# Kernel optimization log

Hardware: AMD Instinct MI355X
Metric: run time of the kernel (lower is better)

Reference implementation:

```python
import jax, jax.numpy as jnp
import numpy as np

N_NODES = 100000
N_EDGES = 1600000
IN_DIM = 128
HEADS = 2
OUT_DIM = 64


def setup_inputs() -> dict:
    key = jax.random.key(0)
    k1, k2, k3, k4, k5 = jax.random.split(key, 5)
    x = jax.random.normal(k1, (N_NODES, IN_DIM), dtype=jnp.float32)
    edge_index = jax.random.randint(k2, (2, N_EDGES), 0, N_NODES, dtype=jnp.int32)
    # xavier-uniform-ish scales
    W = jax.random.uniform(k3, (IN_DIM, HEADS * OUT_DIM), dtype=jnp.float32,
                           minval=-1.0, maxval=1.0) * (6.0 / (IN_DIM + HEADS * OUT_DIM)) ** 0.5
    attn_l = jax.random.uniform(k4, (HEADS, OUT_DIM), dtype=jnp.float32,
                                minval=-1.0, maxval=1.0) * (6.0 / (HEADS + OUT_DIM)) ** 0.5
    attn_r = jax.random.uniform(k5, (HEADS, OUT_DIM), dtype=jnp.float32,
                                minval=-1.0, maxval=1.0) * (6.0 / (HEADS + OUT_DIM)) ** 0.5
    return {"x": x, "edge_index": edge_index, "W": W, "attn_l": attn_l, "attn_r": attn_r}


def reference(x, edge_index, W, attn_l, attn_r):
    N = x.shape[0]
    h = (x @ W).reshape(N, HEADS, OUT_DIM)          # [N,H,D]
    src, dst = edge_index[0], edge_index[1]          # [E]
    h_src = h[src]                                   # [E,H,D] gather
    h_dst = h[dst]                                   # [E,H,D] gather
    # per-edge, per-head attention logits
    alpha = jnp.einsum('ehd,hd->eh', h_src, attn_l) + jnp.einsum('ehd,hd->eh', h_dst, attn_r)
    alpha = jax.nn.leaky_relu(alpha, negative_slope=0.2)
    # NOTE: faithful to original torch code: softmax over dim=0 (ALL edges per head)
    alpha = jax.nn.softmax(alpha, axis=0)            # [E,H]
    msg = h_src * alpha[:, :, None]                  # [E,H,D]
    out = jnp.zeros((N, HEADS, OUT_DIM), dtype=h.dtype).at[dst].add(msg)
    return out.reshape(N, HEADS * OUT_DIM)
```

## Files before the change

### kernel.cpp

```cpp
#include <hip/hip_runtime.h>
#include <hip/hip_fp16.h>
#include <math.h>

#define IN_DIM   128
#define HEADS    2
#define OUT_DIM  64
#define OCOLS    128
#define NB_A     1024
#define BSHIFT   8
#define MAXB     512
#define PCOPIES  8
#define CAP      6144
#define PARTB    128
#define LOG2E    1.4426950408889634f

typedef __attribute__((ext_vector_type(4))) _Float16 half4v;
typedef __attribute__((ext_vector_type(8))) _Float16 half8v;
typedef __attribute__((ext_vector_type(4))) float    floatx4;

__global__ __launch_bounds__(256) void pack_w_kernel(
    const float* __restrict__ W, half8v* __restrict__ wpack) {
  int t = threadIdx.x;
  for (int s = t; s < 2048; s += 256) {
    int l = s & 63, ct = (s >> 6) & 7, kk = s >> 9;
    int q = l >> 4, n = l & 15;
    int c = ct * 16 + n;
    half8v f;
#pragma unroll
    for (int j = 0; j < 8; j++) {
      f[j] = (_Float16)W[(size_t)(kk * 32 + q * 8 + j) * OCOLS + c];
    }
    wpack[s] = f;
  }
}

__global__ __launch_bounds__(256) void gemm_kernel(
    const float* __restrict__ x, const half8v* __restrict__ wpack,
    const float* __restrict__ attn_l, const float* __restrict__ attn_r,
    _Float16* __restrict__ h16, float* __restrict__ alr, int N) {
  __shared__ half8v Wlds[2048];
  __shared__ __align__(16) _Float16 hstage[64 * OCOLS];
  const int tid = threadIdx.x;
  for (int i = tid; i < 2048; i += 256) Wlds[i] = wpack[i];

  const int wave = tid >> 6, lane = tid & 63;
  const int q = lane >> 4, m = lane & 15;
  const int rbase = blockIdx.x * 64 + wave * 16;
  const int arow = rbase + m;
  const bool rok = arow < N;

  half8v a[4];
#pragma unroll
  for (int kk = 0; kk < 4; kk++) {
    float4 u = rok ? *(const float4*)&x[(size_t)arow * IN_DIM + kk * 32 + q * 8]
                   : make_float4(0.f, 0.f, 0.f, 0.f);
    float4 v = rok ? *(const float4*)&x[(size_t)arow * IN_DIM + kk * 32 + q * 8 + 4]
                   : make_float4(0.f, 0.f, 0.f, 0.f);
    a[kk][0] = (_Float16)u.x; a[kk][1] = (_Float16)u.y;
    a[kk][2] = (_Float16)u.z; a[kk][3] = (_Float16)u.w;
    a[kk][4] = (_Float16)v.x; a[kk][5] = (_Float16)v.y;
    a[kk][6] = (_Float16)v.z; a[kk][7] = (_Float16)v.w;
  }
  __syncthreads();

  floatx4 acc[8];
#pragma unroll
  for (int ct = 0; ct < 8; ct++) {
    floatx4 c = {0.f, 0.f, 0.f, 0.f};
#pragma unroll
    for (int kk = 0; kk < 4; kk++) {
      c = __builtin_amdgcn_mfma_f32_16x16x32_f16(
          a[kk], Wlds[(kk * 8 + ct) * 64 + lane], c, 0, 0, 0);
    }
    acc[ct] = c;
  }

  float Al[8], Ar[8];
#pragma unroll
  for (int ct = 0; ct < 8; ct++) {
    Al[ct] = attn_l[ct * 16 + m];
    Ar[ct] = attn_r[ct * 16 + m];
  }
#pragma unroll
  for (int r = 0; r < 4; r++) {
    float al0 = 0.f, al1 = 0.f, ar0 = 0.f, ar1 = 0.f;
#pragma unroll
    for (int ct = 0; ct < 4; ct++) {
      al0 += acc[ct][r] * Al[ct];
      ar0 += acc[ct][r] * Ar[ct];
      al1 += acc[ct + 4][r] * Al[ct + 4];
      ar1 += acc[ct + 4][r] * Ar[ct + 4];
    }
#pragma unroll
    for (int off = 1; off < 16; off <<= 1) {
      al0 += __shfl_xor(al0, off);
      al1 += __shfl_xor(al1, off);
      ar0 += __shfl_xor(ar0, off);
      ar1 += __shfl_xor(ar1, off);
    }
    int orow = rbase + q * 4 + r;
    if (m == 0 && orow < N) {
      *(float4*)&alr[(size_t)orow * 4] =
          make_float4(al0 * LOG2E, al1 * LOG2E, ar0 * LOG2E, ar1 * LOG2E);
    }
  }

#pragma unroll
  for (int ct = 0; ct < 8; ct++) {
#pragma unroll
    for (int r = 0; r < 4; r++) {
      hstage[(wave * 16 + q * 4 + r) * OCOLS + ct * 16 + m] = (_Float16)acc[ct][r];
    }
  }
  __syncthreads();
  {
    int srow = tid >> 2, seg = tid & 3;
    int grow = blockIdx.x * 64 + srow;
    if (grow < N) {
      const int4* s = (const int4*)&hstage[srow * OCOLS + seg * 32];
      int4* d = (int4*)&h16[(size_t)grow * OCOLS + seg * 32];
      int4 v0 = s[0], v1 = s[1], v2 = s[2], v3 = s[3];
      d[0] = v0; d[1] = v1; d[2] = v2; d[3] = v3;
    }
  }
}

__device__ inline void softmax_comb(float& m, float& s, float m2, float s2) {
  float M = fmaxf(m, m2);
  s = s * __builtin_amdgcn_exp2f(m - M) + s2 * __builtin_amdgcn_exp2f(m2 - M);
  m = M;
}

__global__ __launch_bounds__(256) void alpha_stats_kernel(
    const int* __restrict__ src, const int* __restrict__ dst,
    const float* __restrict__ alr, float* __restrict__ partials,
    int* __restrict__ bucket_cnt, int E, int nb1) {
  __shared__ int hist[MAXB];
  for (int i = threadIdx.x; i < MAXB; i += 256) hist[i] = 0;
  __syncthreads();
  const char* ab = (const char*)alr;
  float m0 = -1e30f, s0 = 0.f, m1 = -1e30f, s1 = 0.f;
  for (int e = blockIdx.x * 256 + threadIdx.x; e < E; e += gridDim.x * 256) {
    int sn = src[e], dn = dst[e];
    atomicAdd(&hist[dn >> BSHIFT], 1);
    float4 as = *(const float4*)(ab + ((unsigned)sn << 4));
    float4 ad = *(const float4*)(ab + ((unsigned)dn << 4));
    float a0 = as.x + ad.z;
    float a1 = as.y + ad.w;
    a0 = (a0 > 0.f) ? a0 : 0.2f * a0;
    a1 = (a1 > 0.f) ? a1 : 0.2f * a1;
    {
      float M = fmaxf(m0, a0);
      s0 = s0 * __builtin_amdgcn_exp2f(m0 - M) + __builtin_amdgcn_exp2f(a0 - M);
      m0 = M;
    }
    {
      float M = fmaxf(m1, a1);
      s1 = s1 * __builtin_amdgcn_exp2f(m1 - M) + __builtin_amdgcn_exp2f(a1 - M);
      m1 = M;
    }
  }
  __syncthreads();
  for (int b = threadIdx.x; b < nb1; b += 256) {
    int h = hist[b];
    if (h) atomicAdd(&bucket_cnt[(blockIdx.x & (PCOPIES - 1)) * MAXB + b], h);
  }
#pragma unroll
  for (int off = 1; off < 64; off <<= 1) {
    float m0o = __shfl_xor(m0, off), s0o = __shfl_xor(s0, off);
    float m1o = __shfl_xor(m1, off), s1o = __shfl_xor(s1, off);
    softmax_comb(m0, s0, m0o, s0o);
    softmax_comb(m1, s1, m1o, s1o);
  }
  __shared__ float red[4][4];
  int wave = threadIdx.x >> 6;
  int lane = threadIdx.x & 63;
  if (lane == 0) {
    red[wave][0] = m0; red[wave][1] = s0; red[wave][2] = m1; red[wave][3] = s1;
  }
  __syncthreads();
  if (threadIdx.x == 0) {
    float M0 = red[0][0], S0 = red[0][1], M1 = red[0][2], S1 = red[0][3];
    for (int w = 1; w < 4; w++) {
      softmax_comb(M0, S0, red[w][0], red[w][1]);
      softmax_comb(M1, S1, red[w][2], red[w][3]);
    }
    float* p = &partials[(size_t)blockIdx.x * 4];
    p[0] = M0; p[1] = S0; p[2] = M1; p[3] = S1;
  }
}

__global__ __launch_bounds__(256) void reduce_kernel(
    const float* __restrict__ partials, float* __restrict__ stats) {
  float m0 = -1e30f, s0 = 0.f, m1 = -1e30f, s1 = 0.f;
  for (int i = threadIdx.x; i < NB_A; i += 256) {
    const float* p = &partials[(size_t)i * 4];
    softmax_comb(m0, s0, p[0], p[1]);
    softmax_comb(m1, s1, p[2], p[3]);
  }
#pragma unroll
  for (int off = 1; off < 64; off <<= 1) {
    float m0o = __shfl_xor(m0, off), s0o = __shfl_xor(s0, off);
    float m1o = __shfl_xor(m1, off), s1o = __shfl_xor(s1, off);
    softmax_comb(m0, s0, m0o, s0o);
    softmax_comb(m1, s1, m1o, s1o);
  }
  __shared__ float red[4][4];
  int wave = threadIdx.x >> 6;
  int lane = threadIdx.x & 63;
  if (lane == 0) {
    red[wave][0] = m0; red[wave][1] = s0; red[wave][2] = m1; red[wave][3] = s1;
  }
  __syncthreads();
  if (threadIdx.x == 0) {
    float M0 = red[0][0], S0 = red[0][1], M1 = red[0][2], S1 = red[0][3];
    for (int w = 1; w < 4; w++) {
      softmax_comb(M0, S0, red[w][0], red[w][1]);
      softmax_comb(M1, S1, red[w][2], red[w][3]);
    }
    stats[0] = M0; stats[1] = 1.f / S0;
    stats[2] = M1; stats[3] = 1.f / S1;
  }
}

__global__ __launch_bounds__(512) void bucket_scan_kernel(
    const int* __restrict__ bucket_cnt, int* __restrict__ bucket_off,
    int* __restrict__ bucket_cursor, int nb1) {
  __shared__ int part[512];
  int t = threadIdx.x;
  int v = 0;
  if (t < nb1) {
#pragma unroll
    for (int c = 0; c < PCOPIES; c++) v += bucket_cnt[c * MAXB + t];
  }
  part[t] = v;
  __syncthreads();
  for (int d = 1; d < 512; d <<= 1) {
    int x = (t >= d) ? part[t - d] : 0;
    __syncthreads();
    part[t] += x;
    __syncthreads();
  }
  int excl = part[t] - v;
  if (t < nb1) {
    bucket_off[t] = excl;
    bucket_cursor[t] = excl;
  }
  if (t == 511) bucket_off[nb1] = part[511];
}

__global__ __launch_bounds__(256) void partition_kernel(
    const int* __restrict__ src, const int* __restrict__ dst,
    int* __restrict__ bucket_cursor, unsigned int* __restrict__ pairs,
    int E, int nb1, int chunk) {
  __shared__ int hist[MAXB];
  __shared__ int cur[MAXB];
  int base = blockIdx.x * chunk;
  int lim = min(base + chunk, E);
  for (int i = threadIdx.x; i < MAXB; i += 256) hist[i] = 0;
  __syncthreads();
  for (int e = base + threadIdx.x; e < lim; e += 256) {
    atomicAdd(&hist[dst[e] >> BSHIFT], 1);
  }
  __syncthreads();
  for (int b = threadIdx.x; b < nb1; b += 256) {
    cur[b] = atomicAdd(&bucket_cursor[b], hist[b]);
  }
  __syncthreads();
  for (int e = base + threadIdx.x; e < lim; e += 256) {
    int d = dst[e];
    int slot = atomicAdd(&cur[d >> BSHIFT], 1);
    pairs[slot] = (unsigned int)src[e] | ((unsigned int)(d & 255) << 17);
  }
}

__global__ __launch_bounds__(256) void bucket_csr_kernel(
    const unsigned int* __restrict__ pairs, const int* __restrict__ bucket_off,
    int* __restrict__ off, int* __restrict__ edge_src, int N, int nb1) {
  __shared__ int hist[256];
  __shared__ int cur[256];
  __shared__ int buf[CAP];
  int b = blockIdx.x;
  int t = threadIdx.x;
  int base_node = b << BSHIFT;
  int nn = min(256, N - base_node);
  int pbeg = bucket_off[b], pend = bucket_off[b + 1];
  int cntE = pend - pbeg;

  hist[t] = 0;
  __syncthreads();
  for (int i = t; i < cntE; i += 256) {
    atomicAdd(&hist[pairs[pbeg + i] >> 17], 1);
  }
  __syncthreads();
  int v = hist[t];
  for (int d = 1; d < 256; d <<= 1) {
    int x = (t >= d) ? hist[t - d] : 0;
    __syncthreads();
    hist[t] += x;
    __syncthreads();
  }
  int excl = hist[t] - v;
  cur[t] = excl;
  if (t < nn) off[base_node + t] = pbeg + excl;
  if (b == nb1 - 1 && t == 0) off[N] = pend;
  __syncthreads();
  if (cntE <= CAP) {
    for (int i = t; i < cntE; i += 256) {
      unsigned int p = pairs[pbeg + i];
      int slot = atomicAdd(&cur[p >> 17], 1);
      buf[slot] = (int)(p & 0x1FFFFu);
    }
    __syncthreads();
    for (int i = t; i < cntE; i += 256) {
      edge_src[pbeg + i] = buf[i];
    }
  } else {
    for (int i = t; i < cntE; i += 256) {
      unsigned int p = pairs[pbeg + i];
      int slot = atomicAdd(&cur[p >> 17], 1);
      edge_src[pbeg + slot] = (int)(p & 0x1FFFFu);
    }
  }
}

__global__ __launch_bounds__(256) void gather_kernel(
    const int* __restrict__ off, const int* __restrict__ edge_src,
    const float* __restrict__ alr, const float* __restrict__ stats,
    const _Float16* __restrict__ h16, float* __restrict__ out, int N) {
  int gid = blockIdx.x * 256 + threadIdx.x;
  int n = gid >> 6;
  if (n >= N) return;
  int lane = threadIdx.x & 63;
  int sub = lane >> 4;
  int l = lane & 15;
  int head = l >> 3;

  const char* ab = (const char*)alr;
  const char* hb = (const char*)h16;
  float4 ad = *(const float4*)(ab + ((unsigned)n << 4));
  float adv = head ? ad.w : ad.z;
  float M = stats[head * 2];
  float invS = stats[head * 2 + 1];
  unsigned loff = (unsigned)l * 16u;

  int beg = off[n], end = off[n + 1];
  float acc[8] = {0.f, 0.f, 0.f, 0.f, 0.f, 0.f, 0.f, 0.f};
  int i = beg + sub;
  for (; i + 4 < end; i += 8) {
    int sn0 = edge_src[i], sn1 = edge_src[i + 4];
    float4 as0 = *(const float4*)(ab + ((unsigned)sn0 << 4));
    float4 as1 = *(const float4*)(ab + ((unsigned)sn1 << 4));
    half8v hv0 = *(const half8v*)(hb + (((unsigned)sn0 << 8) + loff));
    half8v hv1 = *(const half8v*)(hb + (((unsigned)sn1 << 8) + loff));
    float a0 = (head ? as0.y : as0.x) + adv;
    float a1 = (head ? as1.y : as1.x) + adv;
    a0 = (a0 > 0.f) ? a0 : 0.2f * a0;
    a1 = (a1 > 0.f) ? a1 : 0.2f * a1;
    float w0 = __builtin_amdgcn_exp2f(a0 - M) * invS;
    float w1 = __builtin_amdgcn_exp2f(a1 - M) * invS;
#pragma unroll
    for (int j = 0; j < 8; j++) acc[j] += w0 * (float)hv0[j];
#pragma unroll
    for (int j = 0; j < 8; j++) acc[j] += w1 * (float)hv1[j];
  }
  if (i < end) {
    int sn = edge_src[i];
    float4 as = *(const float4*)(ab + ((unsigned)sn << 4));
    half8v hv = *(const half8v*)(hb + (((unsigned)sn << 8) + loff));
    float a = (head ? as.y : as.x) + adv;
    a = (a > 0.f) ? a : 0.2f * a;
    float w = __builtin_amdgcn_exp2f(a - M) * invS;
#pragma unroll
    for (int j = 0; j < 8; j++) acc[j] += w * (float)hv[j];
  }
#pragma unroll
  for (int j = 0; j < 8; j++) {
    acc[j] += __shfl_xor(acc[j], 16);
    acc[j] += __shfl_xor(acc[j], 32);
  }
  if (sub == 0) {
    char* ob = (char*)out;
    unsigned obase = ((unsigned)n << 9) + (unsigned)l * 32u;
    *(float4*)(ob + obase)      = make_float4(acc[0], acc[1], acc[2], acc[3]);
    *(float4*)(ob + obase + 16) = make_float4(acc[4], acc[5], acc[6], acc[7]);
  }
}

extern "C" void kernel_launch(void* const* d_in, const int* in_sizes, int n_in,
                              void* d_out, int out_size, void* d_ws, size_t ws_size,
                              hipStream_t stream) {
  const float* x      = (const float*)d_in[0];
  const int*   edge   = (const int*)d_in[1];
  const float* W      = (const float*)d_in[2];
  const float* attn_l = (const float*)d_in[3];
  const float* attn_r = (const float*)d_in[4];

  const int N = in_sizes[0] / IN_DIM;
  const int E = in_sizes[1] / 2;
  const int* src = edge;
  const int* dst = edge + E;
  float* out = (float*)d_out;

  const int nb1 = (N + 255) >> BSHIFT;

  _Float16*     h16      = (_Float16*)d_ws;
  float*        alr      = (float*)(h16 + (size_t)N * OCOLS);
  float*        partials = alr + (size_t)N * 4;
  float*        stats    = partials + (size_t)NB_A * 4;
  int*          bucket_cnt    = (int*)(stats + 4);
  int*          bucket_off    = bucket_cnt + PCOPIES * MAXB;
  int*          bucket_cursor = bucket_off + MAXB + 1;
  int*          off      = bucket_cursor + MAXB;
  unsigned int* pairs    = (unsigned int*)(off + N + 1);
  int*          edge_src = (int*)(pairs + E);
  half8v*       wpack    = (half8v*)(edge_src + E);

  const int chunk = (E + PARTB - 1) / PARTB;

  hipMemsetAsync(bucket_cnt, 0, PCOPIES * MAXB * sizeof(int), stream);

  pack_w_kernel<<<1, 256, 0, stream>>>(W, wpack);
  gemm_kernel<<<(N + 63) / 64, 256, 0, stream>>>(x, wpack, attn_l, attn_r, h16, alr, N);
  alpha_stats_kernel<<<NB_A, 256, 0, stream>>>(src, dst, alr, partials, bucket_cnt, E, nb1);
  reduce_kernel<<<1, 256, 0, stream>>>(partials, stats);
  bucket_scan_kernel<<<1, 512, 0, stream>>>(bucket_cnt, bucket_off, bucket_cursor, nb1);
  partition_kernel<<<PARTB, 256, 0, stream>>>(src, dst, bucket_cursor, pairs, E, nb1, chunk);
  bucket_csr_kernel<<<nb1, 256, 0, stream>>>(pairs, bucket_off, off, edge_src, N, nb1);
  gather_kernel<<<((size_t)N * 64 + 255) / 256, 256, 0, stream>>>(
      off, edge_src, alr, stats, h16, out, N);
}
```

Baseline: 283.4 us.

## Build CSR with per-node degree atomics, two-pass scan, and atomic scatter

Replaces the two-level bucket partition plus per-bucket local sort with a direct CSR build. It counts per-node in-degree with global atomics, runs a two-kernel block scan (the softmax stats reduce is folded into the first scan launch), then scatters edge sources by global atomic cursors. The gather loop is also unrolled to four edges per iteration, and it uses nontemporal loads and stores for edge indices and output. This cuts kernel count and the pairs buffer. In exchange it adds 1.6M global scattered atomics and loses the dst-locality ordering within each node's edge list, which changes the summation order and could hurt gather cache behaviour.

```diff
diff --git a/kernel.cpp b/kernel.cpp
--- a/kernel.cpp
+++ b/kernel.cpp
@@ -7,12 +7,11 @@
 #define OUT_DIM  64
 #define OCOLS    128
 #define NB_A     1024
-#define BSHIFT   8
-#define MAXB     512
-#define PCOPIES  8
-#define CAP      6144
-#define PARTB    128
 #define LOG2E    1.4426950408889634f
+#define SCAN_T   512
+#define SCAN_C   4
+#define SCAN_N   2048
+#define MAXBLK   64
 
 typedef __attribute__((ext_vector_type(4))) _Float16 half4v;
 typedef __attribute__((ext_vector_type(8))) _Float16 half8v;
@@ -134,15 +133,12 @@
 __global__ __launch_bounds__(256) void alpha_stats_kernel(
     const int* __restrict__ src, const int* __restrict__ dst,
     const float* __restrict__ alr, float* __restrict__ partials,
-    int* __restrict__ bucket_cnt, int E, int nb1) {
-  __shared__ int hist[MAXB];
-  for (int i = threadIdx.x; i < MAXB; i += 256) hist[i] = 0;
-  __syncthreads();
+    int* __restrict__ deg, int E) {
   const char* ab = (const char*)alr;
   float m0 = -1e30f, s0 = 0.f, m1 = -1e30f, s1 = 0.f;
   for (int e = blockIdx.x * 256 + threadIdx.x; e < E; e += gridDim.x * 256) {
     int sn = src[e], dn = dst[e];
-    atomicAdd(&hist[dn >> BSHIFT], 1);
+    atomicAdd(&deg[dn], 1);
     float4 as = *(const float4*)(ab + ((unsigned)sn << 4));
     float4 ad = *(const float4*)(ab + ((unsigned)dn << 4));
     float a0 = as.x + ad.z;
@@ -160,11 +156,6 @@
       m1 = M;
     }
   }
-  __syncthreads();
-  for (int b = threadIdx.x; b < nb1; b += 256) {
-    int h = hist[b];
-    if (h) atomicAdd(&bucket_cnt[(blockIdx.x & (PCOPIES - 1)) * MAXB + b], h);
-  }
 #pragma unroll
   for (int off = 1; off < 64; off <<= 1) {
     float m0o = __shfl_xor(m0, off), s0o = __shfl_xor(s0, off);
@@ -190,137 +181,123 @@
   }
 }
 
-__global__ __launch_bounds__(256) void reduce_kernel(
-    const float* __restrict__ partials, float* __restrict__ stats) {
-  float m0 = -1e30f, s0 = 0.f, m1 = -1e30f, s1 = 0.f;
-  for (int i = threadIdx.x; i < NB_A; i += 256) {
-    const float* p = &partials[(size_t)i * 4];
-    softmax_comb(m0, s0, p[0], p[1]);
-    softmax_comb(m1, s1, p[2], p[3]);
-  }
-#pragma unroll
-  for (int off = 1; off < 64; off <<= 1) {
-    float m0o = __shfl_xor(m0, off), s0o = __shfl_xor(s0, off);
-    float m1o = __shfl_xor(m1, off), s1o = __shfl_xor(s1, off);
-    softmax_comb(m0, s0, m0o, s0o);
-    softmax_comb(m1, s1, m1o, s1o);
-  }
-  __shared__ float red[4][4];
-  int wave = threadIdx.x >> 6;
-  int lane = threadIdx.x & 63;
-  if (lane == 0) {
-    red[wave][0] = m0; red[wave][1] = s0; red[wave][2] = m1; red[wave][3] = s1;
-  }
-  __syncthreads();
-  if (threadIdx.x == 0) {
-    float M0 = red[0][0], S0 = red[0][1], M1 = red[0][2], S1 = red[0][3];
-    for (int w = 1; w < 4; w++) {
-      softmax_comb(M0, S0, red[w][0], red[w][1]);
-      softmax_comb(M1, S1, red[w][2], red[w][3]);
-    }
-    stats[0] = M0; stats[1] = 1.f / S0;
-    stats[2] = M1; stats[3] = 1.f / S1;
-  }
-}
-
-__global__ __launch_bounds__(512) void bucket_scan_kernel(
-    const int* __restrict__ bucket_cnt, int* __restrict__ bucket_off,
-    int* __restrict__ bucket_cursor, int nb1) {
+__global__ __launch_bounds__(512) void scan1_kernel(
+    const int* __restrict__ deg, int* __restrict__ bsum,
+    const float* __restrict__ partials, float* __restrict__ stats,
+    int N, int nblk) {
+  __shared__ int ws[8];
+  __shared__ float red[8][4];
+  const int b = blockIdx.x, t = threadIdx.x;
+  const int wave = t >> 6, lane = t & 63;
+
+  if (b == nblk) {
+    float m0 = -1e30f, s0 = 0.f, m1 = -1e30f, s1 = 0.f;
+    for (int i = t; i < NB_A; i += 512) {
+      const float* p = &partials[(size_t)i * 4];
+      softmax_comb(m0, s0, p[0], p[1]);
+      softmax_comb(m1, s1, p[2], p[3]);
+    }
+#pragma unroll
+    for (int off = 1; off < 64; off <<= 1) {
+      float m0o = __shfl_xor(m0, off), s0o = __shfl_xor(s0, off);
+      float m1o = __shfl_xor(m1, off), s1o = __shfl_xor(s1, off);
+      softmax_comb(m0, s0, m0o, s0o);
+      softmax_comb(m1, s1, m1o, s1o);
+    }
+    if (lane == 0) {
+      red[wave][0] = m0; red[wave][1] = s0; red[wave][2] = m1; red[wave][3] = s1;
+    }
+    __syncthreads();
+    if (t == 0) {
+      float M0 = red[0][0], S0 = red[0][1], M1 = red[0][2], S1 = red[0][3];
+      for (int w = 1; w < 8; w++) {
+        softmax_comb(M0, S0, red[w][0], red[w][1]);
+        softmax_comb(M1, S1, red[w][2], red[w][3]);
+      }
+      stats[0] = M0; stats[1] = 1.f / S0;
+      stats[2] = M1; stats[3] = 1.f / S1;
+    }
+    return;
+  }
+
+  int base = b * SCAN_N + t * SCAN_C;
+  int v = 0;
+  if (base + SCAN_C <= N) {
+    int4 d = *(const int4*)&deg[base];
+    v = d.x + d.y + d.z + d.w;
+  } else {
+    for (int j = 0; j < SCAN_C; j++)
+      if (base + j < N) v += deg[base + j];
+  }
+#pragma unroll
+  for (int off = 1; off < 64; off <<= 1) v += __shfl_xor(v, off);
+  if (lane == 0) ws[wave] = v;
+  __syncthreads();
+  if (t == 0) {
+    int s = 0;
+    for (int w = 0; w < 8; w++) s += ws[w];
+    bsum[b] = s;
+  }
+}
+
+__global__ __launch_bounds__(512) void scan2_kernel(
+    const int* __restrict__ deg, const int* __restrict__ bsum,
+    int* __restrict__ off, int* __restrict__ cursor, int N, int nblk, int E) {
+  __shared__ int bs[MAXBLK];
   __shared__ int part[512];
-  int t = threadIdx.x;
-  int v = 0;
-  if (t < nb1) {
-#pragma unroll
-    for (int c = 0; c < PCOPIES; c++) v += bucket_cnt[c * MAXB + t];
-  }
-  part[t] = v;
-  __syncthreads();
-  for (int d = 1; d < 512; d <<= 1) {
-    int x = (t >= d) ? part[t - d] : 0;
+  __shared__ int bpre_s;
+  const int b = blockIdx.x, t = threadIdx.x;
+
+  if (t < MAXBLK) bs[t] = (t < b) ? bsum[t] : 0;
+  __syncthreads();
+  if (t < 64) {
+    int v = bs[t];
+#pragma unroll
+    for (int o = 1; o < 64; o <<= 1) v += __shfl_xor(v, o);
+    if (t == 0) bpre_s = v;
+  }
+
+  int base = b * SCAN_N + t * SCAN_C;
+  int d0 = 0, d1 = 0, d2 = 0, d3 = 0;
+  if (base + SCAN_C <= N) {
+    int4 d = *(const int4*)&deg[base];
+    d0 = d.x; d1 = d.y; d2 = d.z; d3 = d.w;
+  } else {
+    if (base + 0 < N) d0 = deg[base + 0];
+    if (base + 1 < N) d1 = deg[base + 1];
+    if (base + 2 < N) d2 = deg[base + 2];
+    if (base + 3 < N) d3 = deg[base + 3];
+  }
+  int tsum = d0 + d1 + d2 + d3;
+  part[t] = tsum;
+  __syncthreads();
+  for (int dd = 1; dd < 512; dd <<= 1) {
+    int x = (t >= dd) ? part[t - dd] : 0;
     __syncthreads();
     part[t] += x;
     __syncthreads();
   }
-  int excl = part[t] - v;
-  if (t < nb1) {
-    bucket_off[t] = excl;
-    bucket_cursor[t] = excl;
-  }
-  if (t == 511) bucket_off[nb1] = part[511];
-}
-
-__global__ __launch_bounds__(256) void partition_kernel(
+  int excl = part[t] - tsum + bpre_s;
+  int o0 = excl, o1 = o0 + d0, o2 = o1 + d1, o3 = o2 + d2;
+  if (base + SCAN_C <= N) {
+    *(int4*)&off[base]    = make_int4(o0, o1, o2, o3);
+    *(int4*)&cursor[base] = make_int4(o0, o1, o2, o3);
+  } else {
+    if (base + 0 < N) { off[base + 0] = o0; cursor[base + 0] = o0; }
+    if (base + 1 < N) { off[base + 1] = o1; cursor[base + 1] = o1; }
+    if (base + 2 < N) { off[base + 2] = o2; cursor[base + 2] = o2; }
+    if (base + 3 < N) { off[base + 3] = o3; cursor[base + 3] = o3; }
+  }
+  if (b == 0 && t == 0) off[N] = E;
+}
+
+__global__ __launch_bounds__(256) void scatter_kernel(
     const int* __restrict__ src, const int* __restrict__ dst,
-    int* __restrict__ bucket_cursor, unsigned int* __restrict__ pairs,
-    int E, int nb1, int chunk) {
-  __shared__ int hist[MAXB];
-  __shared__ int cur[MAXB];
-  int base = blockIdx.x * chunk;
-  int lim = min(base + chunk, E);
-  for (int i = threadIdx.x; i < MAXB; i += 256) hist[i] = 0;
-  __syncthreads();
-  for (int e = base + threadIdx.x; e < lim; e += 256) {
-    atomicAdd(&hist[dst[e] >> BSHIFT], 1);
-  }
-  __syncthreads();
-  for (int b = threadIdx.x; b < nb1; b += 256) {
-    cur[b] = atomicAdd(&bucket_cursor[b], hist[b]);
-  }
-  __syncthreads();
-  for (int e = base + threadIdx.x; e < lim; e += 256) {
-    int d = dst[e];
-    int slot = atomicAdd(&cur[d >> BSHIFT], 1);
-    pairs[slot] = (unsigned int)src[e] | ((unsigned int)(d & 255) << 17);
-  }
-}
-
-__global__ __launch_bounds__(256) void bucket_csr_kernel(
-    const unsigned int* __restrict__ pairs, const int* __restrict__ bucket_off,
-    int* __restrict__ off, int* __restrict__ edge_src, int N, int nb1) {
-  __shared__ int hist[256];
-  __shared__ int cur[256];
-  __shared__ int buf[CAP];
-  int b = blockIdx.x;
-  int t = threadIdx.x;
-  int base_node = b << BSHIFT;
-  int nn = min(256, N - base_node);
-  int pbeg = bucket_off[b], pend = bucket_off[b + 1];
-  int cntE = pend - pbeg;
-
-  hist[t] = 0;
-  __syncthreads();
-  for (int i = t; i < cntE; i += 256) {
-    atomicAdd(&hist[pairs[pbeg + i] >> 17], 1);
-  }
-  __syncthreads();
-  int v = hist[t];
-  for (int d = 1; d < 256; d <<= 1) {
-    int x = (t >= d) ? hist[t - d] : 0;
-    __syncthreads();
-    hist[t] += x;
-    __syncthreads();
-  }
-  int excl = hist[t] - v;
-  cur[t] = excl;
-  if (t < nn) off[base_node + t] = pbeg + excl;
-  if (b == nb1 - 1 && t == 0) off[N] = pend;
-  __syncthreads();
-  if (cntE <= CAP) {
-    for (int i = t; i < cntE; i += 256) {
-      unsigned int p = pairs[pbeg + i];
-      int slot = atomicAdd(&cur[p >> 17], 1);
-      buf[slot] = (int)(p & 0x1FFFFu);
-    }
-    __syncthreads();
-    for (int i = t; i < cntE; i += 256) {
-      edge_src[pbeg + i] = buf[i];
-    }
-  } else {
-    for (int i = t; i < cntE; i += 256) {
-      unsigned int p = pairs[pbeg + i];
-      int slot = atomicAdd(&cur[p >> 17], 1);
-      edge_src[pbeg + slot] = (int)(p & 0x1FFFFu);
-    }
+    int* __restrict__ cursor, int* __restrict__ edge_src, int E) {
+  for (int e = blockIdx.x * 256 + threadIdx.x; e < E; e += gridDim.x * 256) {
+    int dn = dst[e];
+    int slot = atomicAdd(&cursor[dn], 1);
+    edge_src[slot] = src[e];
   }
 }
 
@@ -347,8 +324,43 @@
   int beg = off[n], end = off[n + 1];
   float acc[8] = {0.f, 0.f, 0.f, 0.f, 0.f, 0.f, 0.f, 0.f};
   int i = beg + sub;
+  for (; i + 12 < end; i += 16) {
+    int sn0 = __builtin_nontemporal_load(&edge_src[i]);
+    int sn1 = __builtin_nontemporal_load(&edge_src[i + 4]);
+    int sn2 = __builtin_nontemporal_load(&edge_src[i + 8]);
+    int sn3 = __builtin_nontemporal_load(&edge_src[i + 12]);
+    float4 as0 = *(const float4*)(ab + ((unsigned)sn0 << 4));
+    float4 as1 = *(const float4*)(ab + ((unsigned)sn1 << 4));
+    float4 as2 = *(const float4*)(ab + ((unsigned)sn2 << 4));
+    float4 as3 = *(const float4*)(ab + ((unsigned)sn3 << 4));
+    half8v hv0 = *(const half8v*)(hb + (((unsigned)sn0 << 8) + loff));
+    half8v hv1 = *(const half8v*)(hb + (((unsigned)sn1 << 8) + loff));
+    half8v hv2 = *(const half8v*)(hb + (((unsigned)sn2 << 8) + loff));
+    half8v hv3 = *(const half8v*)(hb + (((unsigned)sn3 << 8) + loff));
+    float a0 = (head ? as0.y : as0.x) + adv;
+    float a1 = (head ? as1.y : as1.x) + adv;
+    float a2 = (head ? as2.y : as2.x) + adv;
+    float a3 = (head ? as3.y : as3.x) + adv;
+    a0 = (a0 > 0.f) ? a0 : 0.2f * a0;
+    a1 = (a1 > 0.f) ? a1 : 0.2f * a1;
+    a2 = (a2 > 0.f) ? a2 : 0.2f * a2;
+    a3 = (a3 > 0.f) ? a3 : 0.2f * a3;
+    float w0 = __builtin_amdgcn_exp2f(a0 - M) * invS;
+    float w1 = __builtin_amdgcn_exp2f(a1 - M) * invS;
+    float w2 = __builtin_amdgcn_exp2f(a2 - M) * invS;
+    float w3 = __builtin_amdgcn_exp2f(a3 - M) * invS;
+#pragma unroll
+    for (int j = 0; j < 8; j++) acc[j] += w0 * (float)hv0[j];
+#pragma unroll
+    for (int j = 0; j < 8; j++) acc[j] += w1 * (float)hv1[j];
+#pragma unroll
+    for (int j = 0; j < 8; j++) acc[j] += w2 * (float)hv2[j];
+#pragma unroll
+    for (int j = 0; j < 8; j++) acc[j] += w3 * (float)hv3[j];
+  }
   for (; i + 4 < end; i += 8) {
-    int sn0 = edge_src[i], sn1 = edge_src[i + 4];
+    int sn0 = __builtin_nontemporal_load(&edge_src[i]);
+    int sn1 = __builtin_nontemporal_load(&edge_src[i + 4]);
     float4 as0 = *(const float4*)(ab + ((unsigned)sn0 << 4));
     float4 as1 = *(const float4*)(ab + ((unsigned)sn1 << 4));
     half8v hv0 = *(const half8v*)(hb + (((unsigned)sn0 << 8) + loff));
@@ -365,7 +377,7 @@
     for (int j = 0; j < 8; j++) acc[j] += w1 * (float)hv1[j];
   }
   if (i < end) {
-    int sn = edge_src[i];
+    int sn = __builtin_nontemporal_load(&edge_src[i]);
     float4 as = *(const float4*)(ab + ((unsigned)sn << 4));
     half8v hv = *(const half8v*)(hb + (((unsigned)sn << 8) + loff));
     float a = (head ? as.y : as.x) + adv;
@@ -382,8 +394,10 @@
   if (sub == 0) {
     char* ob = (char*)out;
     unsigned obase = ((unsigned)n << 9) + (unsigned)l * 32u;
-    *(float4*)(ob + obase)      = make_float4(acc[0], acc[1], acc[2], acc[3]);
-    *(float4*)(ob + obase + 16) = make_float4(acc[4], acc[5], acc[6], acc[7]);
+    floatx4 o0 = {acc[0], acc[1], acc[2], acc[3]};
+    floatx4 o1 = {acc[4], acc[5], acc[6], acc[7]};
+    __builtin_nontemporal_store(o0, (floatx4*)(ob + obase));
+    __builtin_nontemporal_store(o1, (floatx4*)(ob + obase + 16));
   }
 }
 
@@ -402,31 +416,27 @@
   const int* dst = edge + E;
   float* out = (float*)d_out;
 
-  const int nb1 = (N + 255) >> BSHIFT;
-
-  _Float16*     h16      = (_Float16*)d_ws;
-  float*        alr      = (float*)(h16 + (size_t)N * OCOLS);
-  float*        partials = alr + (size_t)N * 4;
-  float*        stats    = partials + (size_t)NB_A * 4;
-  int*          bucket_cnt    = (int*)(stats + 4);
-  int*          bucket_off    = bucket_cnt + PCOPIES * MAXB;
-  int*          bucket_cursor = bucket_off + MAXB + 1;
-  int*          off      = bucket_cursor + MAXB;
-  unsigned int* pairs    = (unsigned int*)(off + N + 1);
-  int*          edge_src = (int*)(pairs + E);
-  half8v*       wpack    = (half8v*)(edge_src + E);
-
-  const int chunk = (E + PARTB - 1) / PARTB;
-
-  hipMemsetAsync(bucket_cnt, 0, PCOPIES * MAXB * sizeof(int), stream);
+  const int nblk = (N + SCAN_N - 1) / SCAN_N;
+
+  _Float16* h16      = (_Float16*)d_ws;
+  float*    alr      = (float*)(h16 + (size_t)N * OCOLS);
+  float*    partials = alr + (size_t)N * 4;
+  float*    stats    = partials + (size_t)NB_A * 4;
+  int*      deg      = (int*)(stats + 4);
+  int*      bsum     = deg + N;
+  int*      off      = bsum + MAXBLK;
+  int*      cursor   = off + N + 4;
+  int*      edge_src = cursor + N;
+  half8v*   wpack    = (half8v*)(edge_src + E);
+
+  hipMemsetAsync(deg, 0, (size_t)N * sizeof(int), stream);
 
   pack_w_kernel<<<1, 256, 0, stream>>>(W, wpack);
   gemm_kernel<<<(N + 63) / 64, 256, 0, stream>>>(x, wpack, attn_l, attn_r, h16, alr, N);
-  alpha_stats_kernel<<<NB_A, 256, 0, stream>>>(src, dst, alr, partials, bucket_cnt, E, nb1);
-  reduce_kernel<<<1, 256, 0, stream>>>(partials, stats);
-  bucket_scan_kernel<<<1, 512, 0, stream>>>(bucket_cnt, bucket_off, bucket_cursor, nb1);
-  partition_kernel<<<PARTB, 256, 0, stream>>>(src, dst, bucket_cursor, pairs, E, nb1, chunk);
-  bucket_csr_kernel<<<nb1, 256, 0, stream>>>(pairs, bucket_off, off, edge_src, N, nb1);
+  alpha_stats_kernel<<<NB_A, 256, 0, stream>>>(src, dst, alr, partials, deg, E);
+  scan1_kernel<<<nblk + 1, SCAN_T, 0, stream>>>(deg, bsum, partials, stats, N, nblk);
+  scan2_kernel<<<nblk, SCAN_T, 0, stream>>>(deg, bsum, off, cursor, N, nblk, E);
+  scatter_kernel<<<2048, 256, 0, stream>>>(src, dst, cursor, edge_src, E);
   gather_kernel<<<((size_t)N * 64 + 255) / 256, 256, 0, stream>>>(
       off, edge_src, alr, stats, h16, out, N);
 }
```

Result: slower. 394.6 us (+39.2%).
